# Optimization experiments

Measured on AMD Instinct MI355X. Metric: run time of the kernel, lower is better.

## Reference

```python
import jax, jax.numpy as jnp
import numpy as np

B, S, D, H = 2, 2048, 1024, 16
HD = D // H          # 64
HALF = HD // 2       # 32
EPS = 1e-6           # RMSNorm eps (module default eps=1e-6)


def setup_inputs() -> dict:
    key = jax.random.key(0)
    ks = jax.random.split(key, 6)
    x = jax.random.normal(ks[0], (B, S, D), jnp.float32)
    scale = 1.0 / np.sqrt(D)
    Wq = jax.random.normal(ks[1], (D, D), jnp.float32) * scale
    Wk = jax.random.normal(ks[2], (D, D), jnp.float32) * scale
    Wv = jax.random.normal(ks[3], (D, D), jnp.float32) * scale
    Wo = jax.random.normal(ks[4], (D, D), jnp.float32) * scale
    bq = jnp.zeros((D,), jnp.float32)
    bk = jnp.zeros((D,), jnp.float32)
    bv = jnp.zeros((D,), jnp.float32)
    bo = jnp.zeros((D,), jnp.float32)
    gq = jnp.ones((D,), jnp.float32)   # norm_q weight
    gk = jnp.ones((D,), jnp.float32)   # norm_k weight
    # Standard RoPE angles: pos * 10000^(-2i/head_dim); freqs = exp(i*ang)
    pos = jnp.arange(S, dtype=jnp.float32)
    inv_freq = 1.0 / (10000.0 ** (jnp.arange(0, HD, 2, dtype=jnp.float32) / HD))
    ang = pos[:, None] * inv_freq[None, :]          # (S, HALF)
    return dict(x=x, Wq=Wq, bq=bq, Wk=Wk, bk=bk, Wv=Wv, bv=bv, Wo=Wo, bo=bo,
                gq=gq, gk=gk, freqs_cos=jnp.cos(ang), freqs_sin=jnp.sin(ang))


def _rmsnorm(x, g):
    # x * rsqrt(mean(x^2) + eps) * g, computed in fp32 as in the torch module
    return x * jax.lax.rsqrt(jnp.mean(x * x, axis=-1, keepdims=True) + EPS) * g


def _rope(x, cos, sin):
    # x: (B,S,D) packed heads; rotate consecutive (even,odd) pairs per head.
    xr = x.reshape(B, S, H, HALF, 2)
    x0, x1 = xr[..., 0], xr[..., 1]
    c = cos[None, :, None, :]  # (1,S,1,HALF)
    s = sin[None, :, None, :]
    o0 = x0 * c - x1 * s
    o1 = x0 * s + x1 * c
    return jnp.stack([o0, o1], axis=-1).reshape(B, S, D)


def reference(x, Wq, bq, Wk, bk, Wv, bv, Wo, bo, gq, gk, freqs_cos, freqs_sin):
    q = _rmsnorm(x @ Wq.T + bq, gq)
    k = _rmsnorm(x @ Wk.T + bk, gk)
    v = x @ Wv.T + bv
    q = _rope(q, freqs_cos, freqs_sin)
    k = _rope(k, freqs_cos, freqs_sin)
    # SDPA (non-causal, as F.scaled_dot_product_attention default call)
    qh = q.reshape(B, S, H, HD)
    kh = k.reshape(B, S, H, HD)
    vh = v.reshape(B, S, H, HD)
    scores = jnp.einsum('bqhd,bkhd->bhqk', qh, kh) / np.sqrt(HD)
    attn = jax.nn.softmax(scores, axis=-1)
    out = jnp.einsum('bhqk,bkhd->bqhd', attn, vh).reshape(B, S, D)
    return out @ Wo.T + bo
```

## Files before the change

kernel.cpp:

```cpp
#include <hip/hip_runtime.h>

typedef unsigned short u16;
typedef unsigned int u32;
typedef u16 u16x4 __attribute__((ext_vector_type(4)));
typedef u16 u16x8 __attribute__((ext_vector_type(8)));
typedef u32 u32x2 __attribute__((ext_vector_type(2)));
typedef float f32x4 __attribute__((ext_vector_type(4)));
typedef __bf16 bf16x2 __attribute__((ext_vector_type(2)));
typedef __bf16 bf16x8 __attribute__((ext_vector_type(8)));

#define GLOAD16(gp, lp)                                             \
  __builtin_amdgcn_global_load_lds(                                 \
      (const __attribute__((address_space(1))) void*)(gp),          \
      (__attribute__((address_space(3))) void*)(lp), 16, 0, 0)

__device__ __forceinline__ u16 f2bf(float f) {
  unsigned int u = __builtin_bit_cast(unsigned int, f);
  u += 0x7FFFu + ((u >> 16) & 1u);
  return (u16)(u >> 16);
}
__device__ __forceinline__ float bf2f(u16 h) {
  return __builtin_bit_cast(float, (u32)h << 16);
}

__global__ __launch_bounds__(256) void f2b_kernel(const float* __restrict__ in,
                                                  u16* __restrict__ out, int n4) {
  int i = blockIdx.x * 256 + threadIdx.x;
  if (i < n4) {
    f32x4 v = *(const f32x4*)(in + (size_t)i * 4);
    u16x4 o;
    o[0] = f2bf(v[0]); o[1] = f2bf(v[1]); o[2] = f2bf(v[2]); o[3] = f2bf(v[3]);
    *(u16x4*)(out + (size_t)i * 4) = o;
  }
}

__global__ __launch_bounds__(256) void f2bw_kernel(const float* __restrict__ s0,
    const float* __restrict__ s1, const float* __restrict__ s2,
    const float* __restrict__ s3, u16* __restrict__ dst) {
  const int y = blockIdx.y;
  const float* s = (y == 0) ? s0 : ((y == 1) ? s1 : ((y == 2) ? s2 : s3));
  int i = blockIdx.x * 256 + threadIdx.x;
  f32x4 v = *(const f32x4*)(s + (size_t)i * 4);
  u16x4 o;
  o[0] = f2bf(v[0]); o[1] = f2bf(v[1]); o[2] = f2bf(v[2]); o[3] = f2bf(v[3]);
  *(u16x4*)(dst + (size_t)y * 1048576 + (size_t)i * 4) = o;
}

__device__ __forceinline__ void gemm_core(const u16* __restrict__ A,
                                          const u16* __restrict__ W,
                                          int bm0, int bn0,
                                          u16* ldsA, u16* ldsB,
                                          f32x4 acc[4][4]) {
  const int tid = threadIdx.x;
  const int l = tid & 63;
  const int lr = l & 15, lk = l >> 4;
  const int w = tid >> 6;
  const int wr = w >> 1, wc = w & 1;
  const int srow = tid >> 2, sko = (tid & 3) << 3;
  auto stage = [&](int kt, int buf) {
#pragma unroll
    for (int it = 0; it < 2; ++it) {
      int row = it * 64 + srow;
      GLOAD16(A + (size_t)(bm0 + row) * 1024 + kt * 32 + sko,
              ldsA + buf * 4096 + (it * 256 + tid) * 8);
      GLOAD16(W + (size_t)(bn0 + row) * 1024 + kt * 32 + sko,
              ldsB + buf * 4096 + (it * 256 + tid) * 8);
    }
  };
  stage(0, 0);
  stage(1, 1);
  int cur = 0, nx2 = 2;
  for (int kt = 0; kt < 32; ++kt) {
    if (kt < 31) asm volatile("s_waitcnt vmcnt(4)" ::: "memory");
    else         asm volatile("s_waitcnt vmcnt(0)" ::: "memory");
    __builtin_amdgcn_s_barrier();
    __builtin_amdgcn_sched_barrier(0);
    if (kt + 2 < 32) stage(kt + 2, nx2);
    const u16* lA = ldsA + cur * 4096;
    const u16* lB = ldsB + cur * 4096;
    bf16x8 af[4], bfr[4];
#pragma unroll
    for (int m = 0; m < 4; ++m)
      af[m] = *(const bf16x8*)(lA + (wr * 64 + m * 16 + lr) * 32 + lk * 8);
#pragma unroll
    for (int n = 0; n < 4; ++n)
      bfr[n] = *(const bf16x8*)(lB + (wc * 64 + n * 16 + lr) * 32 + lk * 8);
#pragma unroll
    for (int m = 0; m < 4; ++m)
#pragma unroll
      for (int n = 0; n < 4; ++n)
        acc[m][n] = __builtin_amdgcn_mfma_f32_16x16x32_bf16(af[m], bfr[n], acc[m][n], 0, 0, 0);
    cur = (cur == 2) ? 0 : cur + 1;
    nx2 = (nx2 == 2) ? 0 : nx2 + 1;
  }
}

__global__ __launch_bounds__(256) void qkv_gemm(const u16* __restrict__ xb,
    const u16* __restrict__ wq, const u16* __restrict__ wk, const u16* __restrict__ wv,
    const float* __restrict__ bq, const float* __restrict__ bk, const float* __restrict__ bv,
    u16* __restrict__ Qb, u16* __restrict__ Kb, u16* __restrict__ Vt) {
  __shared__ u16 ldsA[3 * 4096];
  __shared__ u16 ldsB[3 * 4096];
  const int z = blockIdx.z;
  const u16* W = (z == 0) ? wq : ((z == 1) ? wk : wv);
  const float* bias = (z == 0) ? bq : ((z == 1) ? bk : bv);
  const int bm0 = blockIdx.x * 128, bn0 = blockIdx.y * 128;
  const f32x4 zf = {0.f, 0.f, 0.f, 0.f};
  f32x4 acc[4][4];
#pragma unroll
  for (int m = 0; m < 4; ++m)
#pragma unroll
    for (int n = 0; n < 4; ++n) acc[m][n] = zf;
  gemm_core(xb, W, bm0, bn0, ldsA, ldsB, acc);
  const int tid = threadIdx.x, l = tid & 63, lr = l & 15, lk = l >> 4;
  const int w = tid >> 6, wr = w >> 1, wc = w & 1;
  float bcol[4];
#pragma unroll
  for (int n = 0; n < 4; ++n) bcol[n] = bias[bn0 + wc * 64 + n * 16 + lr];
  if (z < 2) {
    u16* outp = z ? Kb : Qb;
#pragma unroll
    for (int m = 0; m < 4; ++m)
#pragma unroll
      for (int n = 0; n < 4; ++n)
#pragma unroll
        for (int r = 0; r < 4; ++r) {
          int row = bm0 + wr * 64 + m * 16 + lk * 4 + r;
          int col = bn0 + wc * 64 + n * 16 + lr;
          outp[(size_t)row * 1024 + col] = f2bf(acc[m][n][r] + bcol[n]);
        }
  } else {
#pragma unroll
    for (int m = 0; m < 4; ++m)
#pragma unroll
      for (int n = 0; n < 4; ++n) {
        int row = bm0 + wr * 64 + m * 16 + lk * 4;
        int col = bn0 + wc * 64 + n * 16 + lr;
        int b = row >> 11, s = row & 2047, hh = col >> 6, hd = col & 63;
        u16x4 o;
#pragma unroll
        for (int r = 0; r < 4; ++r) o[r] = f2bf(acc[m][n][r] + bcol[n]);
        *(u16x4*)(Vt + (((size_t)((b * 16 + hh) * 64 + hd)) << 11) + s) = o;
      }
  }
}

__global__ __launch_bounds__(256) void proj_gemm(const u16* __restrict__ ctx,
    const u16* __restrict__ wo, const float* __restrict__ bo, float* __restrict__ out) {
  __shared__ u16 ldsA[3 * 4096];
  __shared__ u16 ldsB[3 * 4096];
  const int bm0 = blockIdx.x * 128, bn0 = blockIdx.y * 128;
  const f32x4 zf = {0.f, 0.f, 0.f, 0.f};
  f32x4 acc[4][4];
#pragma unroll
  for (int m = 0; m < 4; ++m)
#pragma unroll
    for (int n = 0; n < 4; ++n) acc[m][n] = zf;
  gemm_core(ctx, wo, bm0, bn0, ldsA, ldsB, acc);
  const int tid = threadIdx.x, l = tid & 63, lr = l & 15, lk = l >> 4;
  const int w = tid >> 6, wr = w >> 1, wc = w & 1;
  float bcol[4];
#pragma unroll
  for (int n = 0; n < 4; ++n) bcol[n] = bo[bn0 + wc * 64 + n * 16 + lr];
#pragma unroll
  for (int m = 0; m < 4; ++m)
#pragma unroll
    for (int n = 0; n < 4; ++n)
#pragma unroll
      for (int r = 0; r < 4; ++r) {
        int row = bm0 + wr * 64 + m * 16 + lk * 4 + r;
        int col = bn0 + wc * 64 + n * 16 + lr;
        out[(size_t)row * 1024 + col] = acc[m][n][r] + bcol[n];
      }
}

__global__ __launch_bounds__(256) void rmsrope(const u16* __restrict__ Qb,
    const u16* __restrict__ Kb, const float* __restrict__ gq, const float* __restrict__ gk,
    const float* __restrict__ fc, const float* __restrict__ fs,
    u16* __restrict__ Qh, u16* __restrict__ Kh) {
  const int row = blockIdx.x;
  const int which = blockIdx.y;
  const u16* src = (which ? Kb : Qb) + (size_t)row * 1024;
  const float* g = which ? gk : gq;
  u16* dst = which ? Kh : Qh;
  const int t = threadIdx.x;
  u16x4 raw = *(const u16x4*)(src + t * 4);
  float v0 = bf2f(raw[0]), v1 = bf2f(raw[1]), v2 = bf2f(raw[2]), v3 = bf2f(raw[3]);
  float ss = v0 * v0 + v1 * v1 + v2 * v2 + v3 * v3;
#pragma unroll
  for (int mm = 1; mm < 64; mm <<= 1) ss += __shfl_xor(ss, mm);
  __shared__ float red[4];
  if ((t & 63) == 0) red[t >> 6] = ss;
  __syncthreads();
  float rstd = rsqrtf((red[0] + red[1] + red[2] + red[3]) * (1.0f / 1024.0f) + 1e-6f);
  if (!which) rstd *= 0.18033688011112042f;
  int d = t * 4, hh = d >> 6, dh = d & 63, p = dh >> 1;
  int s = row & 2047, b = row >> 11;
  float c0 = fc[(s << 5) + p], s0 = fs[(s << 5) + p];
  float c1 = fc[(s << 5) + p + 1], s1 = fs[(s << 5) + p + 1];
  float x0 = v0 * rstd * g[d];
  float x1 = v1 * rstd * g[d + 1];
  float x2 = v2 * rstd * g[d + 2];
  float x3 = v3 * rstd * g[d + 3];
  u16x4 o;
  o[0] = f2bf(x0 * c0 - x1 * s0);
  o[1] = f2bf(x0 * s0 + x1 * c0);
  o[2] = f2bf(x2 * c1 - x3 * s1);
  o[3] = f2bf(x2 * s1 + x3 * c1);
  *(u16x4*)(dst + ((size_t)((b << 4) + hh) * 2048 + s) * 64 + dh) = o;
}

__global__ __launch_bounds__(512, 4) void attn_kernel(const u16* __restrict__ Qh,
    const u16* __restrict__ Kh, const u16* __restrict__ Vt, u16* __restrict__ ctx) {
  __shared__ u16 Kbuf[3][4096];
  __shared__ u16 Vbuf[3][4096];
  __shared__ __attribute__((aligned(16))) u32 Pl[8][16][36];
  const int tid = threadIdx.x;
  const int w = tid >> 6, l = tid & 63, lr = l & 15, lk = l >> 4;
  const int id = blockIdx.x;
  const int qt = (id >> 3) & 15;
  const int hb = (id & 7) | ((id >> 7) << 3);
  const int h = hb & 15, b = hb >> 4;
  const int bh = b * 16 + h;
  const u16* Q = Qh + (size_t)bh * 2048 * 64;
  const u16* K = Kh + (size_t)bh * 2048 * 64;
  const u16* V = Vt + (size_t)bh * 64 * 2048;
  const int q0 = qt * 128;
  const int srow = tid >> 3;
  const int kslot = (tid & 7) ^ (srow & 7);
  bf16x8 qf[2];
#pragma unroll
  for (int kh = 0; kh < 2; ++kh)
    qf[kh] = *(const bf16x8*)(Q + (size_t)(q0 + w * 16 + lr) * 64 + kh * 32 + lk * 8);
  const f32x4 zf = {0.f, 0.f, 0.f, 0.f};
  f32x4 O[4];
  float Mrun = -1e30f, lsum = 0.f;
#pragma unroll
  for (int n = 0; n < 4; ++n) O[n] = zf;
  GLOAD16(K + ((size_t)srow << 6) + kslot * 8, &Kbuf[0][tid * 8]);
  GLOAD16(V + ((size_t)srow << 11) + kslot * 8, &Vbuf[0][tid * 8]);
  GLOAD16(K + ((size_t)(64 + srow) << 6) + kslot * 8, &Kbuf[1][tid * 8]);
  GLOAD16(V + ((size_t)srow << 11) + 64 + kslot * 8, &Vbuf[1][tid * 8]);
  int cur = 0, nx2 = 2;
  for (int kb = 0; kb < 32; ++kb) {
    if (kb < 31) asm volatile("s_waitcnt vmcnt(2)" ::: "memory");
    else         asm volatile("s_waitcnt vmcnt(0)" ::: "memory");
    __builtin_amdgcn_s_barrier();
    __builtin_amdgcn_sched_barrier(0);
    if (kb + 2 < 32) {
      GLOAD16(K + ((size_t)((kb + 2) * 64 + srow) << 6) + kslot * 8, &Kbuf[nx2][tid * 8]);
      GLOAD16(V + ((size_t)srow << 11) + (kb + 2) * 64 + kslot * 8, &Vbuf[nx2][tid * 8]);
    }
    f32x4 sc[4];
#pragma unroll
    for (int n = 0; n < 4; ++n) sc[n] = zf;
    __builtin_amdgcn_s_setprio(1);
#pragma unroll
    for (int n = 0; n < 4; ++n)
#pragma unroll
      for (int kh = 0; kh < 2; ++kh) {
        bf16x8 kf = *(const bf16x8*)(&Kbuf[cur][(n * 16 + lr) * 64 + (((kh * 4 + lk) ^ (lr & 7)) << 3)]);
        sc[n] = __builtin_amdgcn_mfma_f32_16x16x32_bf16(kf, qf[kh], sc[n], 0, 0, 0);
      }
    __builtin_amdgcn_s_setprio(0);
    float bm = fmaxf(fmaxf(sc[0][0], sc[0][1]), fmaxf(sc[0][2], sc[0][3]));
#pragma unroll
    for (int n = 1; n < 4; ++n)
      bm = fmaxf(bm, fmaxf(fmaxf(sc[n][0], sc[n][1]), fmaxf(sc[n][2], sc[n][3])));
    bm = fmaxf(bm, __shfl_xor(bm, 16));
    bm = fmaxf(bm, __shfl_xor(bm, 32));
    if (!__all(bm <= Mrun + 1.4427f)) {
      float nM = fmaxf(Mrun, bm);
      float f = exp2f(Mrun - nM);
      lsum *= f;
#pragma unroll
      for (int n = 0; n < 4; ++n)
#pragma unroll
        for (int r = 0; r < 4; ++r) O[n][r] *= f;
      Mrun = nM;
    }
    float rs = 0.f;
#pragma unroll
    for (int n = 0; n < 4; ++n) {
      u32 pw[2];
#pragma unroll
      for (int c = 0; c < 2; ++c) {
        float p0 = exp2f(sc[n][2 * c] - Mrun);
        float p1 = exp2f(sc[n][2 * c + 1] - Mrun);
        rs += p0 + p1;
        bf16x2 pp;
        pp[0] = (__bf16)p0; pp[1] = (__bf16)p1;
        pw[c] = __builtin_bit_cast(u32, pp);
      }
      u32x2 pv = {pw[0], pw[1]};
      *(u32x2*)&Pl[w][lr][8 * n + 2 * lk] = pv;
    }
    rs += __shfl_xor(rs, 16);
    rs += __shfl_xor(rs, 32);
    lsum += rs;
    __builtin_amdgcn_s_setprio(1);
#pragma unroll
    for (int kk = 0; kk < 2; ++kk) {
      bf16x8 pa = *(const bf16x8*)&Pl[w][lr][16 * kk + 4 * lk];
#pragma unroll
      for (int n = 0; n < 4; ++n) {
        bf16x8 vb = *(const bf16x8*)(&Vbuf[cur][(n * 16 + lr) * 64 + (((kk * 4 + lk) ^ (lr & 7)) << 3)]);
        O[n] = __builtin_amdgcn_mfma_f32_16x16x32_bf16(vb, pa, O[n], 0, 0, 0);
      }
    }
    __builtin_amdgcn_s_setprio(0);
    cur = (cur == 2) ? 0 : cur + 1;
    nx2 = (nx2 == 2) ? 0 : nx2 + 1;
  }
  float inv = 1.0f / lsum;
  const size_t rowbase = ((size_t)((b << 11) + q0 + w * 16 + lr)) * 1024 + (h << 6);
#pragma unroll
  for (int n = 0; n < 4; ++n) {
    u16x4 o4;
#pragma unroll
    for (int r = 0; r < 4; ++r) o4[r] = f2bf(O[n][r] * inv);
    *(u16x4*)(ctx + rowbase + n * 16 + 4 * lk) = o4;
  }
}

extern "C" void kernel_launch(void* const* d_in, const int* in_sizes, int n_in,
                              void* d_out, int out_size, void* d_ws, size_t ws_size,
                              hipStream_t stream) {
  (void)in_sizes; (void)n_in; (void)out_size; (void)ws_size;
  const float* x  = (const float*)d_in[0];
  const float* Wq = (const float*)d_in[1];
  const float* bq = (const float*)d_in[2];
  const float* Wk = (const float*)d_in[3];
  const float* bk = (const float*)d_in[4];
  const float* Wv = (const float*)d_in[5];
  const float* bv = (const float*)d_in[6];
  const float* Wo = (const float*)d_in[7];
  const float* bo = (const float*)d_in[8];
  const float* gq = (const float*)d_in[9];
  const float* gk = (const float*)d_in[10];
  const float* fc = (const float*)d_in[11];
  const float* fs = (const float*)d_in[12];
  float* out = (float*)d_out;
  char* ws = (char*)d_ws;
  u16*  xb  = (u16*)(ws + 0);
  u16*  wqb = (u16*)(ws + 8388608);
  u16*  wkb = (u16*)(ws + 10485760);
  u16*  wvb = (u16*)(ws + 12582912);
  u16*  wob = (u16*)(ws + 14680064);
  u16*  Qfb = (u16*)(ws + 16777216);
  u16*  Kfb = (u16*)(ws + 25165824);
  u16*  Qhb = (u16*)(ws + 33554432);
  u16*  Khb = (u16*)(ws + 41943040);
  u16*  Vtb = (u16*)(ws + 50331648);
  u16*  ctx = (u16*)(ws + 58720256);

  f2b_kernel<<<4096, 256, 0, stream>>>(x, xb, 1048576);
  f2bw_kernel<<<dim3(1024, 4), 256, 0, stream>>>(Wq, Wk, Wv, Wo, wqb);
  qkv_gemm<<<dim3(32, 8, 3), 256, 0, stream>>>(xb, wqb, wkb, wvb, bq, bk, bv, Qfb, Kfb, Vtb);
  rmsrope<<<dim3(4096, 2), 256, 0, stream>>>(Qfb, Kfb, gq, gk, fc, fs, Qhb, Khb);
  attn_kernel<<<512, 512, 0, stream>>>(Qhb, Khb, Vtb, ctx);
  proj_gemm<<<dim3(32, 8), 256, 0, stream>>>(ctx, wob, bo, out);
}
```

Baseline: 148.0 us.

## Switch attention to 32x32x16 MFMA with register-shuffled P, drop LDS P staging

Restructures the attention kernel so each wave owns 32 query rows and uses 32x32x16 bf16 MFMAs instead of 16x16x32, with 4 waves per block (256 threads) rather than 8. The softmax probabilities are rearranged into the B-operand layout with cross-half lane shuffles instead of being written to and read back from an LDS scratch buffer. The aim is fewer LDS round-trips and fewer K/V fragment loads per FLOP. The cost is higher register pressure and fewer waves per block, so each thread now issues twice as many K/V staging loads.

After: 148.1 us. About the same (+0.1%).

```diff
diff --git a/kernel.cpp b/kernel.cpp
--- a/kernel.cpp
+++ b/kernel.cpp
@@ -5,7 +5,9 @@
 typedef u16 u16x4 __attribute__((ext_vector_type(4)));
 typedef u16 u16x8 __attribute__((ext_vector_type(8)));
 typedef u32 u32x2 __attribute__((ext_vector_type(2)));
+typedef u32 u32x4 __attribute__((ext_vector_type(4)));
 typedef float f32x4 __attribute__((ext_vector_type(4)));
+typedef float f32x16 __attribute__((ext_vector_type(16)));
 typedef __bf16 bf16x2 __attribute__((ext_vector_type(2)));
 typedef __bf16 bf16x8 __attribute__((ext_vector_type(8)));
 
@@ -210,13 +212,14 @@
   *(u16x4*)(dst + ((size_t)((b << 4) + hh) * 2048 + s) * 64 + dh) = o;
 }
 
-__global__ __launch_bounds__(512, 4) void attn_kernel(const u16* __restrict__ Qh,
+__global__ __launch_bounds__(256, 2) void attn_kernel(const u16* __restrict__ Qh,
     const u16* __restrict__ Kh, const u16* __restrict__ Vt, u16* __restrict__ ctx) {
   __shared__ u16 Kbuf[3][4096];
   __shared__ u16 Vbuf[3][4096];
-  __shared__ __attribute__((aligned(16))) u32 Pl[8][16][36];
   const int tid = threadIdx.x;
-  const int w = tid >> 6, l = tid & 63, lr = l & 15, lk = l >> 4;
+  const int w = tid >> 6, l = tid & 63;
+  const int lq = l & 31, hi = l >> 5;
+  const bool hiB = (hi != 0);
   const int id = blockIdx.x;
   const int qt = (id >> 3) & 15;
   const int hb = (id & 7) | ((id >> 7) << 3);
@@ -225,101 +228,124 @@
   const u16* Q = Qh + (size_t)bh * 2048 * 64;
   const u16* K = Kh + (size_t)bh * 2048 * 64;
   const u16* V = Vt + (size_t)bh * 64 * 2048;
-  const int q0 = qt * 128;
-  const int srow = tid >> 3;
-  const int kslot = (tid & 7) ^ (srow & 7);
-  bf16x8 qf[2];
-#pragma unroll
-  for (int kh = 0; kh < 2; ++kh)
-    qf[kh] = *(const bf16x8*)(Q + (size_t)(q0 + w * 16 + lr) * 64 + kh * 32 + lk * 8);
-  const f32x4 zf = {0.f, 0.f, 0.f, 0.f};
-  f32x4 O[4];
+  const int q0 = qt * 128 + w * 32;
+  bf16x8 qf[4];
+#pragma unroll
+  for (int hs = 0; hs < 4; ++hs)
+    qf[hs] = *(const bf16x8*)(Q + (size_t)(q0 + lq) * 64 + hs * 16 + hi * 8);
+  auto stage = [&](int kb, int buf) {
+#pragma unroll
+    for (int it = 0; it < 2; ++it) {
+      int c = it * 256 + tid;
+      int row = c >> 3, gc = (c & 7) ^ (row & 7);
+      GLOAD16(K + ((size_t)(kb * 64 + row) << 6) + gc * 8, &Kbuf[buf][c * 8]);
+      GLOAD16(V + ((size_t)row << 11) + kb * 64 + gc * 8, &Vbuf[buf][c * 8]);
+    }
+  };
+  const f32x16 z16 = {0,0,0,0, 0,0,0,0, 0,0,0,0, 0,0,0,0};
+  f32x16 O0 = z16, O1 = z16;
   float Mrun = -1e30f, lsum = 0.f;
-#pragma unroll
-  for (int n = 0; n < 4; ++n) O[n] = zf;
-  GLOAD16(K + ((size_t)srow << 6) + kslot * 8, &Kbuf[0][tid * 8]);
-  GLOAD16(V + ((size_t)srow << 11) + kslot * 8, &Vbuf[0][tid * 8]);
-  GLOAD16(K + ((size_t)(64 + srow) << 6) + kslot * 8, &Kbuf[1][tid * 8]);
-  GLOAD16(V + ((size_t)srow << 11) + 64 + kslot * 8, &Vbuf[1][tid * 8]);
+  stage(0, 0);
+  stage(1, 1);
   int cur = 0, nx2 = 2;
   for (int kb = 0; kb < 32; ++kb) {
-    if (kb < 31) asm volatile("s_waitcnt vmcnt(2)" ::: "memory");
+    if (kb < 31) asm volatile("s_waitcnt vmcnt(4)" ::: "memory");
     else         asm volatile("s_waitcnt vmcnt(0)" ::: "memory");
     __builtin_amdgcn_s_barrier();
     __builtin_amdgcn_sched_barrier(0);
-    if (kb + 2 < 32) {
-      GLOAD16(K + ((size_t)((kb + 2) * 64 + srow) << 6) + kslot * 8, &Kbuf[nx2][tid * 8]);
-      GLOAD16(V + ((size_t)srow << 11) + (kb + 2) * 64 + kslot * 8, &Vbuf[nx2][tid * 8]);
-    }
-    f32x4 sc[4];
-#pragma unroll
-    for (int n = 0; n < 4; ++n) sc[n] = zf;
+    if (kb + 2 < 32) stage(kb + 2, nx2);
+    const u16* Kb_ = &Kbuf[cur][0];
+    const u16* Vb_ = &Vbuf[cur][0];
+    f32x16 sc0 = z16, sc1 = z16;
     __builtin_amdgcn_s_setprio(1);
 #pragma unroll
-    for (int n = 0; n < 4; ++n)
-#pragma unroll
-      for (int kh = 0; kh < 2; ++kh) {
-        bf16x8 kf = *(const bf16x8*)(&Kbuf[cur][(n * 16 + lr) * 64 + (((kh * 4 + lk) ^ (lr & 7)) << 3)]);
-        sc[n] = __builtin_amdgcn_mfma_f32_16x16x32_bf16(kf, qf[kh], sc[n], 0, 0, 0);
-      }
+    for (int hs = 0; hs < 4; ++hs) {
+      int ch = (hs * 2 + hi) ^ (lq & 7);
+      bf16x8 k0 = *(const bf16x8*)(Kb_ + (lq * 8 + ch) * 8);
+      bf16x8 k1 = *(const bf16x8*)(Kb_ + ((32 + lq) * 8 + ch) * 8);
+      sc0 = __builtin_amdgcn_mfma_f32_32x32x16_bf16(k0, qf[hs], sc0, 0, 0, 0);
+      sc1 = __builtin_amdgcn_mfma_f32_32x32x16_bf16(k1, qf[hs], sc1, 0, 0, 0);
+    }
     __builtin_amdgcn_s_setprio(0);
-    float bm = fmaxf(fmaxf(sc[0][0], sc[0][1]), fmaxf(sc[0][2], sc[0][3]));
-#pragma unroll
-    for (int n = 1; n < 4; ++n)
-      bm = fmaxf(bm, fmaxf(fmaxf(sc[n][0], sc[n][1]), fmaxf(sc[n][2], sc[n][3])));
-    bm = fmaxf(bm, __shfl_xor(bm, 16));
+    float bm = sc0[0];
+#pragma unroll
+    for (int i = 1; i < 16; ++i) bm = fmaxf(bm, sc0[i]);
+#pragma unroll
+    for (int i = 0; i < 16; ++i) bm = fmaxf(bm, sc1[i]);
     bm = fmaxf(bm, __shfl_xor(bm, 32));
     if (!__all(bm <= Mrun + 1.4427f)) {
       float nM = fmaxf(Mrun, bm);
       float f = exp2f(Mrun - nM);
       lsum *= f;
 #pragma unroll
-      for (int n = 0; n < 4; ++n)
-#pragma unroll
-        for (int r = 0; r < 4; ++r) O[n][r] *= f;
+      for (int i = 0; i < 16; ++i) { O0[i] *= f; O1[i] *= f; }
       Mrun = nM;
     }
     float rs = 0.f;
-#pragma unroll
-    for (int n = 0; n < 4; ++n) {
-      u32 pw[2];
-#pragma unroll
-      for (int c = 0; c < 2; ++c) {
-        float p0 = exp2f(sc[n][2 * c] - Mrun);
-        float p1 = exp2f(sc[n][2 * c + 1] - Mrun);
-        rs += p0 + p1;
-        bf16x2 pp;
-        pp[0] = (__bf16)p0; pp[1] = (__bf16)p1;
-        pw[c] = __builtin_bit_cast(u32, pp);
-      }
-      u32x2 pv = {pw[0], pw[1]};
-      *(u32x2*)&Pl[w][lr][8 * n + 2 * lk] = pv;
-    }
-    rs += __shfl_xor(rs, 16);
+    u32 pk0[8], pk1[8];
+#pragma unroll
+    for (int m = 0; m < 8; ++m) {
+      float a0 = exp2f(sc0[2 * m] - Mrun), a1 = exp2f(sc0[2 * m + 1] - Mrun);
+      float c0 = exp2f(sc1[2 * m] - Mrun), c1 = exp2f(sc1[2 * m + 1] - Mrun);
+      rs += (a0 + a1) + (c0 + c1);
+      bf16x2 pA; pA[0] = (__bf16)a0; pA[1] = (__bf16)a1;
+      bf16x2 pC; pC[0] = (__bf16)c0; pC[1] = (__bf16)c1;
+      pk0[m] = __builtin_bit_cast(u32, pA);
+      pk1[m] = __builtin_bit_cast(u32, pC);
+    }
     rs += __shfl_xor(rs, 32);
     lsum += rs;
+    auto xchg = [&](u32 X, u32 Y, u32& wlo, u32& whi) {
+      u32 s1 = hiB ? X : Y;
+      u32 r = (u32)__shfl_xor((int)s1, 32);
+      wlo = hiB ? r : X;
+      whi = hiB ? Y : r;
+    };
+    bf16x8 pb[4];
+    {
+      u32 w0, w1, w2, w3;
+      xchg(pk0[0], pk0[2], w0, w2);
+      xchg(pk0[1], pk0[3], w1, w3);
+      u32x4 pw = {w0, w1, w2, w3};
+      pb[0] = __builtin_bit_cast(bf16x8, pw);
+      xchg(pk0[4], pk0[6], w0, w2);
+      xchg(pk0[5], pk0[7], w1, w3);
+      u32x4 pw1 = {w0, w1, w2, w3};
+      pb[1] = __builtin_bit_cast(bf16x8, pw1);
+      xchg(pk1[0], pk1[2], w0, w2);
+      xchg(pk1[1], pk1[3], w1, w3);
+      u32x4 pw2 = {w0, w1, w2, w3};
+      pb[2] = __builtin_bit_cast(bf16x8, pw2);
+      xchg(pk1[4], pk1[6], w0, w2);
+      xchg(pk1[5], pk1[7], w1, w3);
+      u32x4 pw3 = {w0, w1, w2, w3};
+      pb[3] = __builtin_bit_cast(bf16x8, pw3);
+    }
     __builtin_amdgcn_s_setprio(1);
 #pragma unroll
-    for (int kk = 0; kk < 2; ++kk) {
-      bf16x8 pa = *(const bf16x8*)&Pl[w][lr][16 * kk + 4 * lk];
-#pragma unroll
-      for (int n = 0; n < 4; ++n) {
-        bf16x8 vb = *(const bf16x8*)(&Vbuf[cur][(n * 16 + lr) * 64 + (((kk * 4 + lk) ^ (lr & 7)) << 3)]);
-        O[n] = __builtin_amdgcn_mfma_f32_16x16x32_bf16(vb, pa, O[n], 0, 0, 0);
-      }
+    for (int ks = 0; ks < 4; ++ks) {
+      int cv = (ks * 2 + hi) ^ (lq & 7);
+      bf16x8 v0 = *(const bf16x8*)(Vb_ + (lq * 8 + cv) * 8);
+      bf16x8 v1 = *(const bf16x8*)(Vb_ + ((32 + lq) * 8 + cv) * 8);
+      O0 = __builtin_amdgcn_mfma_f32_32x32x16_bf16(v0, pb[ks], O0, 0, 0, 0);
+      O1 = __builtin_amdgcn_mfma_f32_32x32x16_bf16(v1, pb[ks], O1, 0, 0, 0);
     }
     __builtin_amdgcn_s_setprio(0);
     cur = (cur == 2) ? 0 : cur + 1;
     nx2 = (nx2 == 2) ? 0 : nx2 + 1;
   }
   float inv = 1.0f / lsum;
-  const size_t rowbase = ((size_t)((b << 11) + q0 + w * 16 + lr)) * 1024 + (h << 6);
-#pragma unroll
-  for (int n = 0; n < 4; ++n) {
-    u16x4 o4;
-#pragma unroll
-    for (int r = 0; r < 4; ++r) o4[r] = f2bf(O[n][r] * inv);
-    *(u16x4*)(ctx + rowbase + n * 16 + 4 * lk) = o4;
+  const size_t rowoff = ((size_t)(b * 2048 + q0 + lq)) * 1024 + h * 64;
+#pragma unroll
+  for (int g = 0; g < 4; ++g) {
+    u16x4 oa, ob;
+#pragma unroll
+    for (int rr = 0; rr < 4; ++rr) {
+      oa[rr] = f2bf(O0[4 * g + rr] * inv);
+      ob[rr] = f2bf(O1[4 * g + rr] * inv);
+    }
+    *(u16x4*)(ctx + rowoff + 8 * g + 4 * hi) = oa;
+    *(u16x4*)(ctx + rowoff + 32 + 8 * g + 4 * hi) = ob;
   }
 }
 
@@ -358,6 +384,6 @@
   f2bw_kernel<<<dim3(1024, 4), 256, 0, stream>>>(Wq, Wk, Wv, Wo, wqb);
   qkv_gemm<<<dim3(32, 8, 3), 256, 0, stream>>>(xb, wqb, wkb, wvb, bq, bk, bv, Qfb, Kfb, Vtb);
   rmsrope<<<dim3(4096, 2), 256, 0, stream>>>(Qfb, Kfb, gq, gk, fc, fs, Qhb, Khb);
-  attn_kernel<<<512, 512, 0, stream>>>(Qhb, Khb, Vtb, ctx);
+  attn_kernel<<<512, 256, 0, stream>>>(Qhb, Khb, Vtb, ctx);
   proj_gemm<<<dim3(32, 8), 256, 0, stream>>>(ctx, wob, bo, out);
 }
```
